# Kernel optimization log

Hardware: AMD Instinct MI355X
Metric: run time of the kernel (lower is better)

The kernel has to match this reference:

```python
import jax, jax.numpy as jnp
import numpy as np
import math

B, S, E = 2, 2048, 1024
H, DK, DV = 16, 64, 64


def _rope(q, k):
    # q,k: [B,H,S,D]
    D = q.shape[-1]
    theta = 10000.0 ** (jnp.arange(0, D, 2, dtype=jnp.float32) / D)
    pos = jnp.arange(q.shape[-2], dtype=jnp.float32)
    freqs = pos[:, None] * (1.0 / theta)[None, :]          # [S, D/2]
    emb = jnp.concatenate([freqs, freqs], axis=-1)         # [S, D]
    cos = jnp.cos(emb)[None, None]                          # [1,1,S,D]
    sin = jnp.sin(emb)[None, None]

    def rotate(x):
        x1 = x[..., ::2]
        x2 = x[..., 1::2]
        return jnp.stack([-x2, x1], axis=-1).reshape(x.shape)

    return q * cos + rotate(q) * sin, k * cos + rotate(k) * sin


def setup_inputs() -> dict:
    key = jax.random.key(0)
    ks = jax.random.split(key, 9)
    sE = 1.0 / math.sqrt(E)
    sV = 1.0 / math.sqrt(H * DV)
    return {
        "x": jax.random.normal(ks[0], (B, S, E), dtype=jnp.float32),
        "wq": jax.random.uniform(ks[1], (H * DK, E), jnp.float32, -sE, sE),
        "bq": jax.random.uniform(ks[2], (H * DK,), jnp.float32, -sE, sE),
        "wk": jax.random.uniform(ks[3], (H * DK, E), jnp.float32, -sE, sE),
        "bk": jax.random.uniform(ks[4], (H * DK,), jnp.float32, -sE, sE),
        "wv": jax.random.uniform(ks[5], (H * DV, E), jnp.float32, -sE, sE),
        "bv": jax.random.uniform(ks[6], (H * DV,), jnp.float32, -sE, sE),
        "wo": jax.random.uniform(ks[7], (E, H * DV), jnp.float32, -sV, sV),
        "bo": jax.random.uniform(ks[8], (E,), jnp.float32, -sV, sV),
    }


def reference(x, wq, bq, wk, bk, wv, bv, wo, bo):
    Bx, Sx, Ex = x.shape
    q = (x @ wq.T + bq).reshape(Bx, Sx, H, DK).transpose(0, 2, 1, 3)  # [B,H,S,DK]
    k = (x @ wk.T + bk).reshape(Bx, Sx, H, DK).transpose(0, 2, 1, 3)
    v = (x @ wv.T + bv).reshape(Bx, Sx, H, DV).transpose(0, 2, 1, 3)
    q, k = _rope(q, k)
    scores = jnp.einsum('bhqd,bhkd->bhqk', q, k)  # [B,H,S,S]
    causal = jnp.triu(jnp.ones((Sx, Sx), dtype=bool), k=1)
    scores = jnp.where(causal[None, None], -jnp.inf, scores)
    attn = jax.nn.softmax(scores / math.sqrt(DK), axis=-1)
    out = jnp.einsum('bhqk,bhkd->bhqd', attn, v)  # [B,H,S,DV]
    out = out.transpose(0, 2, 1, 3).reshape(Bx, Sx, H * DV)
    return out @ wo.T + bo
```

## Files before the change

### kernel.cpp

```cpp
#include <hip/hip_runtime.h>

typedef unsigned short u16;
typedef unsigned int u32;
typedef __bf16 bf16x8 __attribute__((ext_vector_type(8)));
typedef float floatx4 __attribute__((ext_vector_type(4)));
typedef float floatx16 __attribute__((ext_vector_type(16)));

#define AS1 __attribute__((address_space(1)))
#define AS3 __attribute__((address_space(3)))

__device__ __forceinline__ u16 f2bf(float f) {
    union { float f; u32 u; } a; a.f = f;
    u32 u = a.u;
    u32 r = (u + 0x7fffu + ((u >> 16) & 1u)) >> 16;
    return (u16)r;
}
__device__ __forceinline__ float bf2f(u16 h) {
    union { u32 u; float f; } a; a.u = ((u32)h) << 16; return a.f;
}
__device__ __forceinline__ u32 cvtpk(float a, float b) {
    u32 d; asm("v_cvt_pk_bf16_f32 %0, %1, %2" : "=v"(d) : "v"(a), "v"(b)); return d;
}
__device__ __forceinline__ void plswap(u32& a, u32& b) {
    asm("v_permlane32_swap_b32 %0, %1" : "+v"(a), "+v"(b));
}

__global__ void k_prep(const float* __restrict__ x,
                       const float* __restrict__ wq, const float* __restrict__ wk,
                       const float* __restrict__ wv, const float* __restrict__ wo,
                       u16* __restrict__ xb, u16* __restrict__ wqb, u16* __restrict__ wkb,
                       u16* __restrict__ wvb, u16* __restrict__ wob,
                       float* __restrict__ ct, float* __restrict__ st) {
    int g = blockIdx.x * blockDim.x + threadIdx.x;
    if (g < 2097152) {
        const float* src; u16* dst; int q;
        if (g < 1048576) { src = x; dst = xb; q = g; }
        else {
            int r = g - 1048576, wsel = r >> 18; q = r & 262143;
            src = (wsel == 0) ? wq : (wsel == 1) ? wk : (wsel == 2) ? wv : wo;
            dst = (wsel == 0) ? wqb : (wsel == 1) ? wkb : (wsel == 2) ? wvb : wob;
        }
        float4 v = reinterpret_cast<const float4*>(src)[q];
        u32 lo = (u32)f2bf(v.x) | ((u32)f2bf(v.y) << 16);
        u32 hi = (u32)f2bf(v.z) | ((u32)f2bf(v.w) << 16);
        reinterpret_cast<uint2*>(dst)[q] = make_uint2(lo, hi);
    } else if (g < 2162688) {
        int i = g - 2097152;
        int s = i >> 5, d = i & 31;
        float inv = powf(10000.f, -(float)d * (1.f / 32.f));
        float ang = (float)s * inv;
        float sv, cv;
        __sincosf(ang, &sv, &cv);
        ct[i] = cv;
        st[i] = sv;
    }
}

__global__ __launch_bounds__(256) void k_gemm_qkv(const u16* __restrict__ A,
        const u16* __restrict__ Wq, const u16* __restrict__ Wk, const u16* __restrict__ Wv,
        const float* __restrict__ Bq, const float* __restrict__ Bk, const float* __restrict__ Bv,
        u16* __restrict__ Oq, u16* __restrict__ Ok, u16* __restrict__ Vt,
        const float* __restrict__ ct, const float* __restrict__ st) {
    __shared__ __attribute__((aligned(16))) u16 Alds[128 * 64];
    __shared__ __attribute__((aligned(16))) u16 Blds[128 * 64];
    const int z = blockIdx.z;
    const u16* __restrict__ W = (z == 0) ? Wq : (z == 1) ? Wk : Wv;
    const float* __restrict__ bias = (z == 0) ? Bq : (z == 1) ? Bk : Bv;
    const int tid = threadIdx.x;
    const int w = tid >> 6, lane = tid & 63;
    const int wr = w >> 1, wc = w & 1;
    const int c = lane & 15, g = lane >> 4;
    const int m0 = blockIdx.y * 128, n0 = blockIdx.x * 128;
    const int K = 1024, N = 1024;
    const int sw = c & 7;
    const int srw = lane >> 3;
    const int scb = (lane & 7) ^ srw;

    floatx4 acc[4][4] = {};

    for (int k0 = 0; k0 < K; k0 += 64) {
        #pragma unroll
        for (int i = 0; i < 4; i++) {
            const int r0 = w * 32 + i * 8;
            const u16* ga = A + (size_t)(m0 + r0 + srw) * K + k0 + scb * 8;
            const u16* gb = W + (size_t)(n0 + r0 + srw) * K + k0 + scb * 8;
            __builtin_amdgcn_global_load_lds((AS1 void*)ga, (AS3 void*)(Alds + r0 * 64), 16, 0, 0);
            __builtin_amdgcn_global_load_lds((AS1 void*)gb, (AS3 void*)(Blds + r0 * 64), 16, 0, 0);
        }
        __syncthreads();
        #pragma unroll
        for (int kk = 0; kk < 2; kk++) {
            bf16x8 af[4], bfr[4];
            const int blk = ((kk * 4 + g) ^ sw) * 8;
            #pragma unroll
            for (int mi = 0; mi < 4; mi++)
                af[mi] = *reinterpret_cast<const bf16x8*>(Alds + (wr * 64 + mi * 16 + c) * 64 + blk);
            #pragma unroll
            for (int ni = 0; ni < 4; ni++)
                bfr[ni] = *reinterpret_cast<const bf16x8*>(Blds + (wc * 64 + ni * 16 + c) * 64 + blk);
            #pragma unroll
            for (int mi = 0; mi < 4; mi++)
                #pragma unroll
                for (int ni = 0; ni < 4; ni++)
                    acc[mi][ni] = __builtin_amdgcn_mfma_f32_16x16x32_bf16(af[mi], bfr[ni], acc[mi][ni], 0, 0, 0);
        }
        __syncthreads();
    }

    if (z < 2) {
        const float SC = 0.125f * 1.44269504088896f;
        u16* __restrict__ Cout = (z == 0) ? Oq : Ok;
        #pragma unroll
        for (int ni = 0; ni < 4; ni++) {
            int col = n0 + wc * 64 + ni * 16 + c;
            int d = col & 63, t = d & 31;
            float sgn = (d & 1) ? 1.f : -1.f;
            float bv = bias[col];
            #pragma unroll
            for (int mi = 0; mi < 4; mi++)
                #pragma unroll
                for (int i = 0; i < 4; i++) {
                    int row = m0 + wr * 64 + mi * 16 + g * 4 + i;
                    int s = row & 2047;
                    float v = acc[mi][ni][i] + bv;
                    float px = __shfl_xor(v, 1);
                    float co = ct[s * 32 + t], si = st[s * 32 + t];
                    float out = v * co + sgn * px * si;
                    if (z == 0) out *= SC;
                    Cout[(size_t)row * N + col] = f2bf(out);
                }
        }
    } else {
        #pragma unroll
        for (int ni = 0; ni < 4; ni++) {
            int col = n0 + wc * 64 + ni * 16 + c;
            float bv = bias[col];
            int hh = col >> 6, d = col & 63;
            #pragma unroll
            for (int mi = 0; mi < 4; mi++) {
                int row0 = m0 + wr * 64 + mi * 16 + g * 4;
                int bb = row0 >> 11, s = row0 & 2047;
                u32 lo = (u32)f2bf(acc[mi][ni][0] + bv) | ((u32)f2bf(acc[mi][ni][1] + bv) << 16);
                u32 hi = (u32)f2bf(acc[mi][ni][2] + bv) | ((u32)f2bf(acc[mi][ni][3] + bv) << 16);
                size_t idx = ((size_t)((bb * 16 + hh) * 64 + d)) * 2048 + s;
                *reinterpret_cast<uint2*>(Vt + idx) = make_uint2(lo, hi);
            }
        }
    }
}

__global__ __launch_bounds__(256) void k_gemm_f32(const u16* __restrict__ A, const u16* __restrict__ W,
                                                  const float* __restrict__ bias, float* __restrict__ Cout) {
    __shared__ __attribute__((aligned(16))) u16 Alds[128 * 64];
    __shared__ __attribute__((aligned(16))) u16 Blds[64 * 64];
    const int tid = threadIdx.x;
    const int w = tid >> 6, lane = tid & 63;
    const int wr = w >> 1, wc = w & 1;
    const int c = lane & 15, g = lane >> 4;
    const int m0 = blockIdx.y * 128, n0 = blockIdx.x * 64;
    const int K = 1024, N = 1024;
    const int sw = c & 7;
    const int srw = lane >> 3;
    const int scb = (lane & 7) ^ srw;

    floatx4 acc[4][2] = {};

    for (int k0 = 0; k0 < K; k0 += 64) {
        #pragma unroll
        for (int i = 0; i < 4; i++) {
            const int r0 = w * 32 + i * 8;
            const u16* ga = A + (size_t)(m0 + r0 + srw) * K + k0 + scb * 8;
            __builtin_amdgcn_global_load_lds((AS1 void*)ga, (AS3 void*)(Alds + r0 * 64), 16, 0, 0);
        }
        #pragma unroll
        for (int i = 0; i < 2; i++) {
            const int r0 = w * 16 + i * 8;
            const u16* gb = W + (size_t)(n0 + r0 + srw) * K + k0 + scb * 8;
            __builtin_amdgcn_global_load_lds((AS1 void*)gb, (AS3 void*)(Blds + r0 * 64), 16, 0, 0);
        }
        __syncthreads();
        #pragma unroll
        for (int kk = 0; kk < 2; kk++) {
            bf16x8 af[4], bfr[2];
            const int blk = ((kk * 4 + g) ^ sw) * 8;
            #pragma unroll
            for (int mi = 0; mi < 4; mi++)
                af[mi] = *reinterpret_cast<const bf16x8*>(Alds + (wr * 64 + mi * 16 + c) * 64 + blk);
            #pragma unroll
            for (int ni = 0; ni < 2; ni++)
                bfr[ni] = *reinterpret_cast<const bf16x8*>(Blds + (wc * 32 + ni * 16 + c) * 64 + blk);
            #pragma unroll
            for (int mi = 0; mi < 4; mi++)
                #pragma unroll
                for (int ni = 0; ni < 2; ni++)
                    acc[mi][ni] = __builtin_amdgcn_mfma_f32_16x16x32_bf16(af[mi], bfr[ni], acc[mi][ni], 0, 0, 0);
        }
        __syncthreads();
    }

    #pragma unroll
    for (int ni = 0; ni < 2; ni++) {
        int col = n0 + wc * 32 + ni * 16 + c;
        float bv = bias[col];
        #pragma unroll
        for (int mi = 0; mi < 4; mi++)
            #pragma unroll
            for (int i = 0; i < 4; i++) {
                int row = m0 + wr * 64 + mi * 16 + g * 4 + i;
                Cout[(size_t)row * N + col] = acc[mi][ni][i] + bv;
            }
    }
}

__global__ __launch_bounds__(512, 4) void k_attn(const u16* __restrict__ Q, const u16* __restrict__ Kg,
                                                 const u16* __restrict__ Vt, u16* __restrict__ O) {
    __shared__ __attribute__((aligned(16))) u16 lds[32768];

    const int tid = threadIdx.x;
    const int w = tid >> 6, lane = tid & 63;
    const int qw = w & 1, kp = w >> 1;
    const int l31 = lane & 31, hi = lane >> 5;
    const int sw = l31 & 7;

    const int id = blockIdx.x;
    const int p = id >> 5;
    const int bh = id & 31;
    const int b = bh >> 4, h = bh & 15;
    const int rowb = b * 2048, colb = h * 64;
    const u16* __restrict__ Kb = Kg + (size_t)rowb * 1024 + colb;
    const u16* __restrict__ Vb = Vt + (size_t)bh * 64 * 2048;
    float* mb = reinterpret_cast<float*>(&lds[0]);

    u16* const Klp = lds + kp * 2 * 2048;
    u16* const Vlp = lds + 16384 + kp * 2 * 2048;

    const int krow8 = lane >> 3;
    const int kblk  = (lane & 7) ^ krow8;
    const int vrow  = (lane & ~7) | ((lane - (lane >> 3)) & 7);
    const int sl0 = (l31 & ~7) | ((l31 + (l31 >> 3)) & 7);
    const int r2x = 32 + l31;
    const int sl1 = (r2x & ~7) | ((r2x + (r2x >> 3)) & 7);

    auto STAGE = [&](int buf, int t) {
        const int kv0 = t * 32;
        if (qw == 0) {
            #pragma unroll
            for (int i = 0; i < 4; i++) {
                const u16* g = Kb + (size_t)(kv0 + i * 8 + krow8) * 1024 + kblk * 8;
                __builtin_amdgcn_global_load_lds((AS1 void*)g, (AS3 void*)(Klp + buf * 2048 + i * 512), 16, 0, 0);
            }
        } else {
            #pragma unroll
            for (int i = 0; i < 4; i++) {
                const u16* g = Vb + (size_t)vrow * 2048 + kv0 + i * 8;
                __builtin_amdgcn_global_load_lds((AS1 void*)g, (AS3 void*)(Vlp + buf * 2048 + i * 512), 16, 0, 0);
            }
        }
    };

    #pragma unroll
    for (int ph = 0; ph < 2; ph++) {
        const int qt = ph ? 31 - p : p;
        const int nt32 = 2 * qt + 2;
        const int NITER = (nt32 + 3) >> 2;
        const int wq0 = qt * 64 + qw * 32;
        const int tmax = 2 * qt + qw;
        const int myq = wq0 + l31;

        bf16x8 qf[4];
        #pragma unroll
        for (int s = 0; s < 4; s++)
            qf[s] = *reinterpret_cast<const bf16x8*>(
                Q + (size_t)(rowb + myq) * 1024 + colb + s * 16 + hi * 8);

        float mreg = -1e30f, ls = 0.f;
        floatx16 acc0 = {}, acc1 = {};

        if (kp < nt32) STAGE(0, kp);
        __syncthreads();

        for (int it = 0; it < NITER; it++) {
            const int bf = it & 1;
            const int t = kp + 4 * it;
            if (t + 4 < nt32) STAGE(bf ^ 1, t + 4);

            if (t < nt32 && t <= tmax) {
                const int kv0 = t * 32;
                floatx16 st4 = {};
                __builtin_amdgcn_s_setprio(1);
                #pragma unroll
                for (int s = 0; s < 4; s++) {
                    bf16x8 kf = *reinterpret_cast<const bf16x8*>(
                        Klp + bf * 2048 + l31 * 64 + (((s * 2 + hi) ^ sw) << 3));
                    st4 = __builtin_amdgcn_mfma_f32_32x32x16_bf16(kf, qf[s], st4, 0, 0, 0);
                }
                __builtin_amdgcn_s_setprio(0);

                float pv[16];
                const bool diag = (kv0 + 31 > wq0);
                #pragma unroll
                for (int rr = 0; rr < 16; rr++) {
                    float sv = st4[rr];
                    if (diag) {
                        int kv = kv0 + (rr & 3) + 8 * (rr >> 2) + 4 * hi;
                        if (kv > myq) sv = -1e30f;
                    }
                    pv[rr] = sv;
                }
                float x0 = fmaxf(fmaxf(pv[0], pv[1]), pv[2]);
                float x1 = fmaxf(fmaxf(pv[3], pv[4]), pv[5]);
                float x2 = fmaxf(fmaxf(pv[6], pv[7]), pv[8]);
                float x3 = fmaxf(fmaxf(pv[9], pv[10]), pv[11]);
                float x4 = fmaxf(fmaxf(pv[12], pv[13]), pv[14]);
                float pm = fmaxf(fmaxf(fmaxf(x0, x1), x2), fmaxf(fmaxf(x3, x4), pv[15]));
                pm = fmaxf(pm, __shfl_xor(pm, 32));
                if (__any(pm > mreg + 8.f)) {
                    float mn = fmaxf(mreg, pm);
                    float corr = exp2f(mreg - mn);
                    mreg = mn;
                    ls *= corr;
                    acc0 *= corr;
                    acc1 *= corr;
                }
                #pragma unroll
                for (int rr = 0; rr < 16; rr++) pv[rr] = exp2f(pv[rr] - mreg);
                float sm = ((pv[0] + pv[1]) + (pv[2] + pv[3])) + ((pv[4] + pv[5]) + (pv[6] + pv[7]))
                         + ((pv[8] + pv[9]) + (pv[10] + pv[11])) + ((pv[12] + pv[13]) + (pv[14] + pv[15]));
                sm += __shfl_xor(sm, 32);
                ls += sm;

                union { u32 u[4]; bf16x8 v; } f0, f1;
                {
                    u32 a0 = cvtpk(pv[0], pv[1]), b0 = cvtpk(pv[4], pv[5]);
                    u32 c0 = cvtpk(pv[2], pv[3]), d0 = cvtpk(pv[6], pv[7]);
                    plswap(a0, b0); plswap(c0, d0);
                    f0.u[0] = a0; f0.u[1] = c0; f0.u[2] = b0; f0.u[3] = d0;
                    u32 e1 = cvtpk(pv[8], pv[9]),  g1 = cvtpk(pv[12], pv[13]);
                    u32 h1 = cvtpk(pv[10], pv[11]), i1 = cvtpk(pv[14], pv[15]);
                    plswap(e1, g1); plswap(h1, i1);
                    f1.u[0] = e1; f1.u[1] = h1; f1.u[2] = g1; f1.u[3] = i1;
                }
                __builtin_amdgcn_s_setprio(1);
                #pragma unroll
                for (int s = 0; s < 2; s++) {
                    const int bcol = s * 2 + hi;
                    bf16x8 v0 = *reinterpret_cast<const bf16x8*>(Vlp + bf * 2048 + ((bcol << 6) + sl0) * 8);
                    bf16x8 v1 = *reinterpret_cast<const bf16x8*>(Vlp + bf * 2048 + ((bcol << 6) + sl1) * 8);
                    const bf16x8 pf = (s == 0) ? f0.v : f1.v;
                    acc0 = __builtin_amdgcn_mfma_f32_32x32x16_bf16(v0, pf, acc0, 0, 0, 0);
                    acc1 = __builtin_amdgcn_mfma_f32_32x32x16_bf16(v1, pf, acc1, 0, 0, 0);
                }
                __builtin_amdgcn_s_setprio(0);
            }
            __syncthreads();
        }

        if (kp > 0) {
            const int base = ((kp - 1) * 2 + qw) * 34 * 64;
            #pragma unroll
            for (int j = 0; j < 16; j++) {
                mb[base + j * 64 + lane] = acc0[j];
                mb[base + (16 + j) * 64 + lane] = acc1[j];
            }
            mb[base + 32 * 64 + lane] = mreg;
            mb[base + 33 * 64 + lane] = ls;
        }
        __syncthreads();
        if (kp == 0) {
            float me[3], le[3];
            #pragma unroll
            for (int e = 0; e < 3; e++) {
                const int base = (e * 2 + qw) * 34 * 64;
                me[e] = mb[base + 32 * 64 + lane];
                le[e] = mb[base + 33 * 64 + lane];
            }
            float mn = fmaxf(fmaxf(mreg, me[0]), fmaxf(me[1], me[2]));
            float c0 = exp2f(mreg - mn);
            float ce[3];
            #pragma unroll
            for (int e = 0; e < 3; e++) ce[e] = exp2f(me[e] - mn);
            float lsm = ls * c0 + le[0] * ce[0] + le[1] * ce[1] + le[2] * ce[2];
            float inv = 1.f / lsm;
            u16* __restrict__ Orow = O + (size_t)(rowb + myq) * 1024 + colb;
            #pragma unroll
            for (int db = 0; db < 2; db++) {
                const floatx16& a = db ? acc1 : acc0;
                #pragma unroll
                for (int g4 = 0; g4 < 4; g4++) {
                    float vv[4];
                    #pragma unroll
                    for (int i = 0; i < 4; i++) {
                        const int row = db * 16 + g4 * 4 + i;
                        float acc = a[g4 * 4 + i] * c0;
                        #pragma unroll
                        for (int e = 0; e < 3; e++)
                            acc += mb[((e * 2 + qw) * 34 + row) * 64 + lane] * ce[e];
                        vv[i] = acc * inv;
                    }
                    u32 lo = cvtpk(vv[0], vv[1]), hh = cvtpk(vv[2], vv[3]);
                    *reinterpret_cast<uint2*>(Orow + db * 32 + g4 * 8 + hi * 4) = make_uint2(lo, hh);
                }
            }
        }
        __syncthreads();
    }
}

extern "C" void kernel_launch(void* const* d_in, const int* in_sizes, int n_in,
                              void* d_out, int out_size, void* d_ws, size_t ws_size,
                              hipStream_t stream) {
    const float* x  = (const float*)d_in[0];
    const float* wq = (const float*)d_in[1];
    const float* bq = (const float*)d_in[2];
    const float* wk = (const float*)d_in[3];
    const float* bk = (const float*)d_in[4];
    const float* wv = (const float*)d_in[5];
    const float* bv = (const float*)d_in[6];
    const float* wo = (const float*)d_in[7];
    const float* bo = (const float*)d_in[8];

    char* ws = (char*)d_ws;
    u16* xb  = (u16*)(ws);
    u16* wqb = (u16*)(ws + (8ull  << 20));
    u16* wkb = (u16*)(ws + (10ull << 20));
    u16* wvb = (u16*)(ws + (12ull << 20));
    u16* wob = (u16*)(ws + (14ull << 20));
    u16* qg  = (u16*)(ws + (16ull << 20));
    u16* kg  = (u16*)(ws + (24ull << 20));
    u16* vt  = (u16*)(ws + (32ull << 20));
    u16* og  = (u16*)(ws + (40ull << 20));
    float* ct = (float*)(ws + (48ull << 20));
    float* st = (float*)(ws + (49ull << 20));

    k_prep<<<8448, 256, 0, stream>>>(x, wq, wk, wv, wo, xb, wqb, wkb, wvb, wob, ct, st);

    dim3 gq(8, 32, 3);
    k_gemm_qkv<<<gq, 256, 0, stream>>>(xb, wqb, wkb, wvb, bq, bk, bv, qg, kg, vt, ct, st);

    k_attn<<<512, 512, 0, stream>>>(qg, kg, vt, og);

    k_gemm_f32<<<dim3(16, 32), 256, 0, stream>>>(og, wob, bo, (float*)d_out);
}
```

Before: 126.5 us.

## Double-buffer LDS in projection GEMMs and use 8 waves for QKV GEMM

Both the QKV and output projection GEMMs now keep two LDS stages, so the next K-tile's global-to-LDS load is issued before the MFMAs on the current tile run, with one barrier per step. The QKV GEMM also moves to 512 threads in a 2x4 wave grid, with each wave computing a 64x32 sub-tile. The aim is to hide global load latency and raise the number of waves per CU. The cost is double the LDS per block, which can lower how many blocks fit on a CU. The QKV epilogue is re-indexed to match the new wave layout.

```diff
diff --git a/kernel.cpp b/kernel.cpp
--- a/kernel.cpp
+++ b/kernel.cpp
@@ -56,52 +56,60 @@
     }
 }
 
-__global__ __launch_bounds__(256) void k_gemm_qkv(const u16* __restrict__ A,
+__global__ __launch_bounds__(512, 4) void k_gemm_qkv(const u16* __restrict__ A,
         const u16* __restrict__ Wq, const u16* __restrict__ Wk, const u16* __restrict__ Wv,
         const float* __restrict__ Bq, const float* __restrict__ Bk, const float* __restrict__ Bv,
         u16* __restrict__ Oq, u16* __restrict__ Ok, u16* __restrict__ Vt,
         const float* __restrict__ ct, const float* __restrict__ st) {
-    __shared__ __attribute__((aligned(16))) u16 Alds[128 * 64];
-    __shared__ __attribute__((aligned(16))) u16 Blds[128 * 64];
+    __shared__ __attribute__((aligned(16))) u16 Alds[2 * 128 * 64];
+    __shared__ __attribute__((aligned(16))) u16 Blds[2 * 128 * 64];
     const int z = blockIdx.z;
     const u16* __restrict__ W = (z == 0) ? Wq : (z == 1) ? Wk : Wv;
     const float* __restrict__ bias = (z == 0) ? Bq : (z == 1) ? Bk : Bv;
     const int tid = threadIdx.x;
     const int w = tid >> 6, lane = tid & 63;
-    const int wr = w >> 1, wc = w & 1;
+    const int wr = w >> 2, wc = w & 3;
     const int c = lane & 15, g = lane >> 4;
     const int m0 = blockIdx.y * 128, n0 = blockIdx.x * 128;
     const int K = 1024, N = 1024;
     const int sw = c & 7;
-    const int srw = lane >> 3;
-    const int scb = (lane & 7) ^ srw;
-
-    floatx4 acc[4][4] = {};
-
-    for (int k0 = 0; k0 < K; k0 += 64) {
-        #pragma unroll
-        for (int i = 0; i < 4; i++) {
-            const int r0 = w * 32 + i * 8;
-            const u16* ga = A + (size_t)(m0 + r0 + srw) * K + k0 + scb * 8;
-            const u16* gb = W + (size_t)(n0 + r0 + srw) * K + k0 + scb * 8;
-            __builtin_amdgcn_global_load_lds((AS1 void*)ga, (AS3 void*)(Alds + r0 * 64), 16, 0, 0);
-            __builtin_amdgcn_global_load_lds((AS1 void*)gb, (AS3 void*)(Blds + r0 * 64), 16, 0, 0);
-        }
-        __syncthreads();
+    const int srw8 = lane >> 3;
+    const int scb = (lane & 7) ^ srw8;
+
+    floatx4 acc[4][2] = {};
+
+    auto STAGE = [&](int buf, int step) {
+        const int k0 = step * 64;
+        #pragma unroll
+        for (int i = 0; i < 2; i++) {
+            const int r0 = w * 16 + i * 8;
+            const u16* ga = A + (size_t)(m0 + r0 + srw8) * K + k0 + scb * 8;
+            const u16* gb = W + (size_t)(n0 + r0 + srw8) * K + k0 + scb * 8;
+            __builtin_amdgcn_global_load_lds((AS1 void*)ga, (AS3 void*)(Alds + buf * 8192 + r0 * 64), 16, 0, 0);
+            __builtin_amdgcn_global_load_lds((AS1 void*)gb, (AS3 void*)(Blds + buf * 8192 + r0 * 64), 16, 0, 0);
+        }
+    };
+
+    STAGE(0, 0);
+    __syncthreads();
+
+    for (int step = 0; step < 16; step++) {
+        const int buf = step & 1;
+        if (step + 1 < 16) STAGE(buf ^ 1, step + 1);
         #pragma unroll
         for (int kk = 0; kk < 2; kk++) {
-            bf16x8 af[4], bfr[4];
+            bf16x8 af[4], bfr[2];
             const int blk = ((kk * 4 + g) ^ sw) * 8;
             #pragma unroll
             for (int mi = 0; mi < 4; mi++)
-                af[mi] = *reinterpret_cast<const bf16x8*>(Alds + (wr * 64 + mi * 16 + c) * 64 + blk);
-            #pragma unroll
-            for (int ni = 0; ni < 4; ni++)
-                bfr[ni] = *reinterpret_cast<const bf16x8*>(Blds + (wc * 64 + ni * 16 + c) * 64 + blk);
+                af[mi] = *reinterpret_cast<const bf16x8*>(Alds + buf * 8192 + (wr * 64 + mi * 16 + c) * 64 + blk);
+            #pragma unroll
+            for (int ni = 0; ni < 2; ni++)
+                bfr[ni] = *reinterpret_cast<const bf16x8*>(Blds + buf * 8192 + (wc * 32 + ni * 16 + c) * 64 + blk);
             #pragma unroll
             for (int mi = 0; mi < 4; mi++)
                 #pragma unroll
-                for (int ni = 0; ni < 4; ni++)
+                for (int ni = 0; ni < 2; ni++)
                     acc[mi][ni] = __builtin_amdgcn_mfma_f32_16x16x32_bf16(af[mi], bfr[ni], acc[mi][ni], 0, 0, 0);
         }
         __syncthreads();
@@ -111,8 +119,8 @@
         const float SC = 0.125f * 1.44269504088896f;
         u16* __restrict__ Cout = (z == 0) ? Oq : Ok;
         #pragma unroll
-        for (int ni = 0; ni < 4; ni++) {
-            int col = n0 + wc * 64 + ni * 16 + c;
+        for (int ni = 0; ni < 2; ni++) {
+            int col = n0 + wc * 32 + ni * 16 + c;
             int d = col & 63, t = d & 31;
             float sgn = (d & 1) ? 1.f : -1.f;
             float bv = bias[col];
@@ -132,8 +140,8 @@
         }
     } else {
         #pragma unroll
-        for (int ni = 0; ni < 4; ni++) {
-            int col = n0 + wc * 64 + ni * 16 + c;
+        for (int ni = 0; ni < 2; ni++) {
+            int col = n0 + wc * 32 + ni * 16 + c;
             float bv = bias[col];
             int hh = col >> 6, d = col & 63;
             #pragma unroll
@@ -151,8 +159,8 @@
 
 __global__ __launch_bounds__(256) void k_gemm_f32(const u16* __restrict__ A, const u16* __restrict__ W,
                                                   const float* __restrict__ bias, float* __restrict__ Cout) {
-    __shared__ __attribute__((aligned(16))) u16 Alds[128 * 64];
-    __shared__ __attribute__((aligned(16))) u16 Blds[64 * 64];
+    __shared__ __attribute__((aligned(16))) u16 Alds[2 * 128 * 64];
+    __shared__ __attribute__((aligned(16))) u16 Blds[2 * 64 * 64];
     const int tid = threadIdx.x;
     const int w = tid >> 6, lane = tid & 63;
     const int wr = w >> 1, wc = w & 1;
@@ -160,35 +168,43 @@
     const int m0 = blockIdx.y * 128, n0 = blockIdx.x * 64;
     const int K = 1024, N = 1024;
     const int sw = c & 7;
-    const int srw = lane >> 3;
-    const int scb = (lane & 7) ^ srw;
+    const int srw8 = lane >> 3;
+    const int scb = (lane & 7) ^ srw8;
 
     floatx4 acc[4][2] = {};
 
-    for (int k0 = 0; k0 < K; k0 += 64) {
+    auto STAGE = [&](int buf, int step) {
+        const int k0 = step * 64;
         #pragma unroll
         for (int i = 0; i < 4; i++) {
             const int r0 = w * 32 + i * 8;
-            const u16* ga = A + (size_t)(m0 + r0 + srw) * K + k0 + scb * 8;
-            __builtin_amdgcn_global_load_lds((AS1 void*)ga, (AS3 void*)(Alds + r0 * 64), 16, 0, 0);
+            const u16* ga = A + (size_t)(m0 + r0 + srw8) * K + k0 + scb * 8;
+            __builtin_amdgcn_global_load_lds((AS1 void*)ga, (AS3 void*)(Alds + buf * 8192 + r0 * 64), 16, 0, 0);
         }
         #pragma unroll
         for (int i = 0; i < 2; i++) {
             const int r0 = w * 16 + i * 8;
-            const u16* gb = W + (size_t)(n0 + r0 + srw) * K + k0 + scb * 8;
-            __builtin_amdgcn_global_load_lds((AS1 void*)gb, (AS3 void*)(Blds + r0 * 64), 16, 0, 0);
-        }
-        __syncthreads();
+            const u16* gb = W + (size_t)(n0 + r0 + srw8) * K + k0 + scb * 8;
+            __builtin_amdgcn_global_load_lds((AS1 void*)gb, (AS3 void*)(Blds + buf * 4096 + r0 * 64), 16, 0, 0);
+        }
+    };
+
+    STAGE(0, 0);
+    __syncthreads();
+
+    for (int step = 0; step < 16; step++) {
+        const int buf = step & 1;
+        if (step + 1 < 16) STAGE(buf ^ 1, step + 1);
         #pragma unroll
         for (int kk = 0; kk < 2; kk++) {
             bf16x8 af[4], bfr[2];
             const int blk = ((kk * 4 + g) ^ sw) * 8;
             #pragma unroll
             for (int mi = 0; mi < 4; mi++)
-                af[mi] = *reinterpret_cast<const bf16x8*>(Alds + (wr * 64 + mi * 16 + c) * 64 + blk);
+                af[mi] = *reinterpret_cast<const bf16x8*>(Alds + buf * 8192 + (wr * 64 + mi * 16 + c) * 64 + blk);
             #pragma unroll
             for (int ni = 0; ni < 2; ni++)
-                bfr[ni] = *reinterpret_cast<const bf16x8*>(Blds + (wc * 32 + ni * 16 + c) * 64 + blk);
+                bfr[ni] = *reinterpret_cast<const bf16x8*>(Blds + buf * 4096 + (wc * 32 + ni * 16 + c) * 64 + blk);
             #pragma unroll
             for (int mi = 0; mi < 4; mi++)
                 #pragma unroll
@@ -435,7 +451,7 @@
     k_prep<<<8448, 256, 0, stream>>>(x, wq, wk, wv, wo, xb, wqb, wkb, wvb, wob, ct, st);
 
     dim3 gq(8, 32, 3);
-    k_gemm_qkv<<<gq, 256, 0, stream>>>(xb, wqb, wkb, wvb, bq, bk, bv, qg, kg, vt, ct, st);
+    k_gemm_qkv<<<gq, 512, 0, stream>>>(xb, wqb, wkb, wvb, bq, bk, bv, qg, kg, vt, ct, st);
 
     k_attn<<<512, 512, 0, stream>>>(qg, kg, vt, og);
 
```

New measurement: 129.7 us. 1.03x slower.

## Fuse Q, K, V projections into one block sharing the activation tile

Applied to the files above, without the earlier changes.

The QKV GEMM used to launch a separate grid slice per projection, so each slice reloaded the same activation tile. Now each block loads one 64-row activation tile and multiplies it against all three weight tiles, keeping three sets of accumulators, and the RoPE/scale and transposed-V epilogues run in the same block. This removes the repeated activation loads but shrinks the M tile. It also raises LDS use to about 56KB and triples accumulator registers, which may cut occupancy.

```diff
diff --git a/kernel.cpp b/kernel.cpp
--- a/kernel.cpp
+++ b/kernel.cpp
@@ -61,90 +61,99 @@
         const float* __restrict__ Bq, const float* __restrict__ Bk, const float* __restrict__ Bv,
         u16* __restrict__ Oq, u16* __restrict__ Ok, u16* __restrict__ Vt,
         const float* __restrict__ ct, const float* __restrict__ st) {
-    __shared__ __attribute__((aligned(16))) u16 Alds[128 * 64];
-    __shared__ __attribute__((aligned(16))) u16 Blds[128 * 64];
-    const int z = blockIdx.z;
-    const u16* __restrict__ W = (z == 0) ? Wq : (z == 1) ? Wk : Wv;
-    const float* __restrict__ bias = (z == 0) ? Bq : (z == 1) ? Bk : Bv;
+    __shared__ __attribute__((aligned(16))) u16 Alds[64 * 64];
+    __shared__ __attribute__((aligned(16))) u16 Wlds[3 * 128 * 64];
     const int tid = threadIdx.x;
     const int w = tid >> 6, lane = tid & 63;
     const int wr = w >> 1, wc = w & 1;
     const int c = lane & 15, g = lane >> 4;
-    const int m0 = blockIdx.y * 128, n0 = blockIdx.x * 128;
+    const int m0 = blockIdx.y * 64, n0 = blockIdx.x * 128;
     const int K = 1024, N = 1024;
     const int sw = c & 7;
-    const int srw = lane >> 3;
-    const int scb = (lane & 7) ^ srw;
-
-    floatx4 acc[4][4] = {};
+    const int srw8 = lane >> 3;
+    const int scb = (lane & 7) ^ srw8;
+
+    floatx4 aq[2][4] = {}, ak[2][4] = {}, av[2][4] = {};
 
     for (int k0 = 0; k0 < K; k0 += 64) {
         #pragma unroll
-        for (int i = 0; i < 4; i++) {
-            const int r0 = w * 32 + i * 8;
-            const u16* ga = A + (size_t)(m0 + r0 + srw) * K + k0 + scb * 8;
-            const u16* gb = W + (size_t)(n0 + r0 + srw) * K + k0 + scb * 8;
+        for (int i = 0; i < 2; i++) {
+            const int r0 = w * 16 + i * 8;
+            const u16* ga = A + (size_t)(m0 + r0 + srw8) * K + k0 + scb * 8;
             __builtin_amdgcn_global_load_lds((AS1 void*)ga, (AS3 void*)(Alds + r0 * 64), 16, 0, 0);
-            __builtin_amdgcn_global_load_lds((AS1 void*)gb, (AS3 void*)(Blds + r0 * 64), 16, 0, 0);
+        }
+        #pragma unroll
+        for (int z3 = 0; z3 < 3; z3++) {
+            const u16* Wz = (z3 == 0) ? Wq : (z3 == 1) ? Wk : Wv;
+            #pragma unroll
+            for (int i = 0; i < 4; i++) {
+                const int r0 = w * 32 + i * 8;
+                const u16* gb = Wz + (size_t)(n0 + r0 + srw8) * K + k0 + scb * 8;
+                __builtin_amdgcn_global_load_lds((AS1 void*)gb, (AS3 void*)(Wlds + z3 * 8192 + r0 * 64), 16, 0, 0);
+            }
         }
         __syncthreads();
         #pragma unroll
         for (int kk = 0; kk < 2; kk++) {
-            bf16x8 af[4], bfr[4];
             const int blk = ((kk * 4 + g) ^ sw) * 8;
-            #pragma unroll
-            for (int mi = 0; mi < 4; mi++)
-                af[mi] = *reinterpret_cast<const bf16x8*>(Alds + (wr * 64 + mi * 16 + c) * 64 + blk);
-            #pragma unroll
-            for (int ni = 0; ni < 4; ni++)
-                bfr[ni] = *reinterpret_cast<const bf16x8*>(Blds + (wc * 64 + ni * 16 + c) * 64 + blk);
-            #pragma unroll
-            for (int mi = 0; mi < 4; mi++)
+            bf16x8 af[2];
+            #pragma unroll
+            for (int mi = 0; mi < 2; mi++)
+                af[mi] = *reinterpret_cast<const bf16x8*>(Alds + (wr * 32 + mi * 16 + c) * 64 + blk);
+            #pragma unroll
+            for (int z3 = 0; z3 < 3; z3++) {
+                bf16x8 bfr[4];
                 #pragma unroll
                 for (int ni = 0; ni < 4; ni++)
-                    acc[mi][ni] = __builtin_amdgcn_mfma_f32_16x16x32_bf16(af[mi], bfr[ni], acc[mi][ni], 0, 0, 0);
-        }
-        __syncthreads();
-    }
-
-    if (z < 2) {
-        const float SC = 0.125f * 1.44269504088896f;
-        u16* __restrict__ Cout = (z == 0) ? Oq : Ok;
-        #pragma unroll
-        for (int ni = 0; ni < 4; ni++) {
-            int col = n0 + wc * 64 + ni * 16 + c;
-            int d = col & 63, t = d & 31;
-            float sgn = (d & 1) ? 1.f : -1.f;
-            float bv = bias[col];
-            #pragma unroll
-            for (int mi = 0; mi < 4; mi++)
-                #pragma unroll
-                for (int i = 0; i < 4; i++) {
-                    int row = m0 + wr * 64 + mi * 16 + g * 4 + i;
-                    int s = row & 2047;
-                    float v = acc[mi][ni][i] + bv;
-                    float px = __shfl_xor(v, 1);
-                    float co = ct[s * 32 + t], si = st[s * 32 + t];
-                    float out = v * co + sgn * px * si;
-                    if (z == 0) out *= SC;
-                    Cout[(size_t)row * N + col] = f2bf(out);
-                }
-        }
-    } else {
-        #pragma unroll
-        for (int ni = 0; ni < 4; ni++) {
-            int col = n0 + wc * 64 + ni * 16 + c;
-            float bv = bias[col];
-            int hh = col >> 6, d = col & 63;
-            #pragma unroll
-            for (int mi = 0; mi < 4; mi++) {
-                int row0 = m0 + wr * 64 + mi * 16 + g * 4;
-                int bb = row0 >> 11, s = row0 & 2047;
-                u32 lo = (u32)f2bf(acc[mi][ni][0] + bv) | ((u32)f2bf(acc[mi][ni][1] + bv) << 16);
-                u32 hi = (u32)f2bf(acc[mi][ni][2] + bv) | ((u32)f2bf(acc[mi][ni][3] + bv) << 16);
-                size_t idx = ((size_t)((bb * 16 + hh) * 64 + d)) * 2048 + s;
-                *reinterpret_cast<uint2*>(Vt + idx) = make_uint2(lo, hi);
-            }
+                    bfr[ni] = *reinterpret_cast<const bf16x8*>(Wlds + z3 * 8192 + (wc * 64 + ni * 16 + c) * 64 + blk);
+                #pragma unroll
+                for (int mi = 0; mi < 2; mi++)
+                    #pragma unroll
+                    for (int ni = 0; ni < 4; ni++) {
+                        if (z3 == 0) aq[mi][ni] = __builtin_amdgcn_mfma_f32_16x16x32_bf16(af[mi], bfr[ni], aq[mi][ni], 0, 0, 0);
+                        if (z3 == 1) ak[mi][ni] = __builtin_amdgcn_mfma_f32_16x16x32_bf16(af[mi], bfr[ni], ak[mi][ni], 0, 0, 0);
+                        if (z3 == 2) av[mi][ni] = __builtin_amdgcn_mfma_f32_16x16x32_bf16(af[mi], bfr[ni], av[mi][ni], 0, 0, 0);
+                    }
+            }
+        }
+        __syncthreads();
+    }
+
+    const float SC = 0.125f * 1.44269504088896f;
+    #pragma unroll
+    for (int ni = 0; ni < 4; ni++) {
+        int col = n0 + wc * 64 + ni * 16 + c;
+        int d = col & 63, t = d & 31;
+        float sgn = (d & 1) ? 1.f : -1.f;
+        float bvq = Bq[col], bvk = Bk[col];
+        #pragma unroll
+        for (int mi = 0; mi < 2; mi++)
+            #pragma unroll
+            for (int i = 0; i < 4; i++) {
+                int row = m0 + wr * 32 + mi * 16 + g * 4 + i;
+                int s = row & 2047;
+                float co = ct[s * 32 + t], si = st[s * 32 + t];
+                float vq = aq[mi][ni][i] + bvq;
+                float pq = __shfl_xor(vq, 1);
+                Oq[(size_t)row * N + col] = f2bf((vq * co + sgn * pq * si) * SC);
+                float vk = ak[mi][ni][i] + bvk;
+                float pk = __shfl_xor(vk, 1);
+                Ok[(size_t)row * N + col] = f2bf(vk * co + sgn * pk * si);
+            }
+    }
+    #pragma unroll
+    for (int ni = 0; ni < 4; ni++) {
+        int col = n0 + wc * 64 + ni * 16 + c;
+        float bv = Bv[col];
+        int hh = col >> 6, d = col & 63;
+        #pragma unroll
+        for (int mi = 0; mi < 2; mi++) {
+            int row0 = m0 + wr * 32 + mi * 16 + g * 4;
+            int bb = row0 >> 11, s = row0 & 2047;
+            u32 lo = (u32)f2bf(av[mi][ni][0] + bv) | ((u32)f2bf(av[mi][ni][1] + bv) << 16);
+            u32 hi = (u32)f2bf(av[mi][ni][2] + bv) | ((u32)f2bf(av[mi][ni][3] + bv) << 16);
+            size_t idx = ((size_t)((bb * 16 + hh) * 64 + d)) * 2048 + s;
+            *reinterpret_cast<uint2*>(Vt + idx) = make_uint2(lo, hi);
         }
     }
 }
@@ -160,8 +169,8 @@
     const int m0 = blockIdx.y * 128, n0 = blockIdx.x * 64;
     const int K = 1024, N = 1024;
     const int sw = c & 7;
-    const int srw = lane >> 3;
-    const int scb = (lane & 7) ^ srw;
+    const int srw8 = lane >> 3;
+    const int scb = (lane & 7) ^ srw8;
 
     floatx4 acc[4][2] = {};
 
@@ -169,13 +178,13 @@
         #pragma unroll
         for (int i = 0; i < 4; i++) {
             const int r0 = w * 32 + i * 8;
-            const u16* ga = A + (size_t)(m0 + r0 + srw) * K + k0 + scb * 8;
+            const u16* ga = A + (size_t)(m0 + r0 + srw8) * K + k0 + scb * 8;
             __builtin_amdgcn_global_load_lds((AS1 void*)ga, (AS3 void*)(Alds + r0 * 64), 16, 0, 0);
         }
         #pragma unroll
         for (int i = 0; i < 2; i++) {
             const int r0 = w * 16 + i * 8;
-            const u16* gb = W + (size_t)(n0 + r0 + srw) * K + k0 + scb * 8;
+            const u16* gb = W + (size_t)(n0 + r0 + srw8) * K + k0 + scb * 8;
             __builtin_amdgcn_global_load_lds((AS1 void*)gb, (AS3 void*)(Blds + r0 * 64), 16, 0, 0);
         }
         __syncthreads();
@@ -434,7 +443,7 @@
 
     k_prep<<<8448, 256, 0, stream>>>(x, wq, wk, wv, wo, xb, wqb, wkb, wvb, wob, ct, st);
 
-    dim3 gq(8, 32, 3);
+    dim3 gq(8, 64);
     k_gemm_qkv<<<gq, 256, 0, stream>>>(xb, wqb, wkb, wvb, bq, bk, bv, qg, kg, vt, ct, st);
 
     k_attn<<<512, 512, 0, stream>>>(qg, kg, vt, og);
```

Measured after the change: 142.2 us. 12.4% more time.
